# Kernel optimization log

Measured on AMD Instinct MI355X. Metric: run time of the kernel, lower is better.

## Reference

```python
import jax, jax.numpy as jnp
import numpy as np

D_MODEL = 512
N_HEADS = 8
D_FF = 2048
EPS = 1e-5


def _layernorm(x, g, b):
    mu = jnp.mean(x, axis=-1, keepdims=True)
    var = jnp.mean(jnp.square(x - mu), axis=-1, keepdims=True)
    return (x - mu) * jax.lax.rsqrt(var + EPS) * g + b


def setup_inputs() -> dict:
    key = jax.random.key(0)
    ks = jax.random.split(key, 12)
    B, N, C = 2, 2048, D_MODEL
    s = lambda fi, fo: 1.0 / np.sqrt(fi)
    inp = {
        "x": jax.random.normal(ks[0], (B, N, C), jnp.float32),
        # weights stored as [in, out] (y = x @ W + b)
        "qkv_w": jax.random.normal(ks[1], (C, 3 * C), jnp.float32) * s(C, 3 * C),
        "qkv_b": jnp.zeros((3 * C,), jnp.float32),
        "out_w": jax.random.normal(ks[2], (C, C), jnp.float32) * s(C, C),
        "out_b": jnp.zeros((C,), jnp.float32),
        "ffn_w1": jax.random.normal(ks[3], (C, D_FF), jnp.float32) * s(C, D_FF),
        "ffn_b1": jnp.zeros((D_FF,), jnp.float32),
        "ffn_w2": jax.random.normal(ks[4], (D_FF, C), jnp.float32) * s(D_FF, C),
        "ffn_b2": jnp.zeros((C,), jnp.float32),
        "n1_g": jnp.ones((C,), jnp.float32),
        "n1_b": jnp.zeros((C,), jnp.float32),
        "n2_g": jnp.ones((C,), jnp.float32),
        "n2_b": jnp.zeros((C,), jnp.float32),
        "conv_w": jax.random.normal(ks[5], (C, C, 3), jnp.float32) * s(3 * C, C),  # [out, in, k]
        "conv_b": jnp.zeros((C,), jnp.float32),
        "cn_g": jnp.ones((C,), jnp.float32),
        "cn_b": jnp.zeros((C,), jnp.float32),
    }
    return inp


def _forward(x, qkv_w, qkv_b, out_w, out_b, ffn_w1, ffn_b1, ffn_w2, ffn_b2,
             n1_g, n1_b, n2_g, n2_b, conv_w, conv_b, cn_g, cn_b):
    B, N, C = x.shape
    H, dk = N_HEADS, C // N_HEADS
    scale = 1.0 / np.sqrt(dk)

    # --- ProbSparse self-attention ---
    qkv = (x @ qkv_w + qkv_b).reshape(B, N, 3, H, dk)
    q, k, v = (jnp.moveaxis(qkv, (2, 3), (0, 2))[i] for i in range(3))  # each [B,H,N,dk]
    scores = jnp.einsum("bhnd,bhmd->bhnm", q, k) * scale  # [B,H,N,N]
    M = jnp.max(scores, axis=-1) - jnp.mean(scores, axis=-1)  # [B,H,N]
    n_top = max(1, min(int(N * 0.25), N - 1))
    _, top_idx = jax.lax.top_k(M, n_top)  # [B,H,n_top]
    bidx = jnp.arange(B)[:, None, None]
    hidx = jnp.arange(H)[None, :, None]
    row_sel = jnp.zeros((B, H, N), bool).at[bidx, hidx, top_idx].set(True)
    # rows not selected are fully masked (-1e9) -> uniform softmax, as in the original
    attn = jax.nn.softmax(jnp.where(row_sel[..., None], scores, -1e9), axis=-1)
    out = jnp.einsum("bhnm,bhmd->bhnd", attn, v)
    out = out.transpose(0, 2, 1, 3).reshape(B, N, C)
    attn_out = out @ out_w + out_b

    x = _layernorm(x + attn_out, n1_g, n1_b)

    # --- FFN (exact GELU) ---
    h = jax.nn.gelu(x @ ffn_w1 + ffn_b1, approximate=False)
    ffn_out = h @ ffn_w2 + ffn_b2
    x = _layernorm(x + ffn_out, n2_g, n2_b)

    # --- distilling conv: circular conv1d(k=3,p=1) -> maxpool(k=3,s=2,p=1) -> ELU -> LN ---
    xc = x.transpose(0, 2, 1)  # [B,C,N]
    xc = jnp.concatenate([xc[..., -1:], xc, xc[..., :1]], axis=-1)  # circular pad 1
    xc = jax.lax.conv_general_dilated(
        xc, conv_w, window_strides=(1,), padding="VALID",
        dimension_numbers=("NCH", "OIH", "NCH")) + conv_b[None, :, None]
    # maxpool k=3 s=2 p=1 (pad with -inf)
    neg = jnp.finfo(xc.dtype).min
    xc = jax.lax.reduce_window(xc, neg, jax.lax.max,
                               window_dimensions=(1, 1, 3), window_strides=(1, 1, 2),
                               padding=((0, 0), (0, 0), (1, 1)))
    x = xc.transpose(0, 2, 1)  # [B, N', C]
    x = _layernorm(jax.nn.elu(x), cn_g, cn_b)
    return x


def reference(x, qkv_w, qkv_b, out_w, out_b, ffn_w1, ffn_b1, ffn_w2, ffn_b2,
              n1_g, n1_b, n2_g, n2_b, conv_w, conv_b, cn_g, cn_b):
    return _forward(x, qkv_w, qkv_b, out_w, out_b, ffn_w1, ffn_b1, ffn_w2, ffn_b2,
                    n1_g, n1_b, n2_g, n2_b, conv_w, conv_b, cn_g, cn_b)
```

## Files before the change

### kernel.cpp

```cpp
#include <hip/hip_runtime.h>
#include <math.h>

#define NB 2
#define NN 2048
#define NC 512
#define NH 8
#define DK 64
#define DFF 2048
#define NTOP 512
#define NPOOL 1024
#define KSPLIT 4

typedef unsigned short u16;
typedef __attribute__((ext_vector_type(8))) short frag8;
typedef __attribute__((ext_vector_type(8))) _Float16 h8;
typedef __attribute__((ext_vector_type(4))) float f32x4;

static __device__ __forceinline__ u16 f2b(float f) {
    union { float f; unsigned int u; } v; v.f = f;
    unsigned int r = (v.u + 0x7fffu + ((v.u >> 16) & 1u)) >> 16;
    return (u16)r;
}
static __device__ __forceinline__ float b2f(u16 v) {
    union { unsigned u; float f; } x; x.u = ((unsigned)v) << 16; return x.f;
}
static __device__ __forceinline__ u16 f2h_bits(float f) {
    union { _Float16 h; u16 u; } v; v.h = (_Float16)f; return v.u;
}
static __device__ __forceinline__ float h2f_bits(u16 u) {
    union { u16 u; _Float16 h; } v; v.u = u; return (float)v.h;
}

template<int MODE>
__global__ __launch_bounds__(256) void mfma_gemm(const u16* __restrict__ A, int lda,
    const u16* __restrict__ Bt, const float* __restrict__ bias,
    float* __restrict__ C, u16* __restrict__ Cb, int ldc, int K, int act)
{
    __shared__ u16 As[128][72];
    __shared__ u16 Bs[128][72];
    int tid = threadIdx.x;
    int m0 = blockIdx.x * 128, n0 = blockIdx.y * 128;
    int wave = tid >> 6, lane = tid & 63;
    int ln = lane & 15, quad = lane >> 4;
    int wm = (wave >> 1) * 64, wn = (wave & 1) * 64;
    f32x4 acc[4][4] = {};
    for (int k0 = 0; k0 < K; k0 += 64) {
        #pragma unroll
        for (int i = 0; i < 4; i++) {
            int t = tid + i * 256;
            int m = t >> 3, kq = t & 7;
            size_t aoff;
            if (MODE == 1) {
                int grow = m0 + m;
                int shift = (k0 >> 9) - 1;
                int arow = (grow & ~(NN - 1)) | ((grow + shift) & (NN - 1));
                aoff = (size_t)arow * NC + ((k0 & 511) + kq * 8);
            } else {
                aoff = (size_t)(m0 + m) * lda + k0 + kq * 8;
            }
            *(uint4*)&As[m][kq * 8] = *(const uint4*)&A[aoff];
            *(uint4*)&Bs[m][kq * 8] = *(const uint4*)&Bt[(size_t)(n0 + m) * K + k0 + kq * 8];
        }
        __syncthreads();
        #pragma unroll
        for (int kk = 0; kk < 2; kk++) {
            frag8 af[4], bf[4];
            #pragma unroll
            for (int i = 0; i < 4; i++) {
                af[i] = *(const frag8*)&As[wm + i * 16 + ln][kk * 32 + quad * 8];
                bf[i] = *(const frag8*)&Bs[wn + i * 16 + ln][kk * 32 + quad * 8];
            }
            #pragma unroll
            for (int i = 0; i < 4; i++)
                #pragma unroll
                for (int j = 0; j < 4; j++)
                    acc[i][j] = __builtin_amdgcn_mfma_f32_16x16x32_bf16(
                        af[i], bf[j], acc[i][j], 0, 0, 0);
        }
        __syncthreads();
    }
    #pragma unroll
    for (int i = 0; i < 4; i++) {
        #pragma unroll
        for (int j = 0; j < 4; j++) {
            int col = n0 + wn + j * 16 + ln;
            float bv = bias ? bias[col] : 0.f;
            #pragma unroll
            for (int r = 0; r < 4; r++) {
                int row = m0 + wm + i * 16 + quad * 4 + r;
                float v = acc[i][j][r] + bv;
                if (act == 1) v = 0.5f * v * (1.0f + erff(v * 0.70710678118654752f));
                if (Cb) Cb[(size_t)row * ldc + col] = f2b(v);
                else    C[(size_t)row * ldc + col] = v;
            }
        }
    }
}

template<int MODE>
__global__ __launch_bounds__(256) void mfma_gemm_sk(const u16* __restrict__ A, int lda,
    const u16* __restrict__ Bt, float* __restrict__ P0, float* __restrict__ P1,
    int ldc, int K)
{
    __shared__ u16 As[128][72];
    __shared__ u16 Bs[128][72];
    int tid = threadIdx.x;
    int m0 = blockIdx.x * 128, n0 = blockIdx.y * 128;
    int split = blockIdx.z;
    int K2 = K >> 1, kbeg = split * K2;
    int wave = tid >> 6, lane = tid & 63;
    int ln = lane & 15, quad = lane >> 4;
    int wm = (wave >> 1) * 64, wn = (wave & 1) * 64;
    f32x4 acc[4][4] = {};
    for (int k0 = kbeg; k0 < kbeg + K2; k0 += 64) {
        #pragma unroll
        for (int i = 0; i < 4; i++) {
            int t = tid + i * 256;
            int m = t >> 3, kq = t & 7;
            size_t aoff;
            if (MODE == 1) {
                int grow = m0 + m;
                int shift = (k0 >> 9) - 1;
                int arow = (grow & ~(NN - 1)) | ((grow + shift) & (NN - 1));
                aoff = (size_t)arow * NC + ((k0 & 511) + kq * 8);
            } else {
                aoff = (size_t)(m0 + m) * lda + k0 + kq * 8;
            }
            *(uint4*)&As[m][kq * 8] = *(const uint4*)&A[aoff];
            *(uint4*)&Bs[m][kq * 8] = *(const uint4*)&Bt[(size_t)(n0 + m) * K + k0 + kq * 8];
        }
        __syncthreads();
        #pragma unroll
        for (int kk = 0; kk < 2; kk++) {
            frag8 af[4], bf[4];
            #pragma unroll
            for (int i = 0; i < 4; i++) {
                af[i] = *(const frag8*)&As[wm + i * 16 + ln][kk * 32 + quad * 8];
                bf[i] = *(const frag8*)&Bs[wn + i * 16 + ln][kk * 32 + quad * 8];
            }
            #pragma unroll
            for (int i = 0; i < 4; i++)
                #pragma unroll
                for (int j = 0; j < 4; j++)
                    acc[i][j] = __builtin_amdgcn_mfma_f32_16x16x32_bf16(
                        af[i], bf[j], acc[i][j], 0, 0, 0);
        }
        __syncthreads();
    }
    float* P = split ? P1 : P0;
    #pragma unroll
    for (int i = 0; i < 4; i++) {
        #pragma unroll
        for (int j = 0; j < 4; j++) {
            int col = n0 + wn + j * 16 + ln;
            #pragma unroll
            for (int r = 0; r < 4; r++) {
                int row = m0 + wm + i * 16 + quad * 4 + r;
                P[(size_t)row * ldc + col] = acc[i][j][r];
            }
        }
    }
}

__global__ __launch_bounds__(256) void mfma_qkv(const u16* __restrict__ A,
    const u16* __restrict__ Bt, const float* __restrict__ bias,
    u16* __restrict__ Qbs, u16* __restrict__ Kb, float* __restrict__ Vh,
    u16* __restrict__ Qcat, u16* __restrict__ Kcat)
{
    __shared__ u16 As[128][72];
    __shared__ u16 Bs[128][72];
    int tid = threadIdx.x;
    int m0 = blockIdx.x * 128, n0 = blockIdx.y * 128;
    int wave = tid >> 6, lane = tid & 63;
    int ln = lane & 15, quad = lane >> 4;
    int wm = (wave >> 1) * 64, wn = (wave & 1) * 64;
    f32x4 acc[4][4] = {};
    for (int k0 = 0; k0 < 1024; k0 += 64) {
        #pragma unroll
        for (int i = 0; i < 4; i++) {
            int t = tid + i * 256;
            int m = t >> 3, kq = t & 7;
            *(uint4*)&As[m][kq * 8] = *(const uint4*)&A[(size_t)(m0 + m) * 1024 + k0 + kq * 8];
            *(uint4*)&Bs[m][kq * 8] = *(const uint4*)&Bt[(size_t)(n0 + m) * 1024 + k0 + kq * 8];
        }
        __syncthreads();
        #pragma unroll
        for (int kk = 0; kk < 2; kk++) {
            h8 af[4], bf[4];
            #pragma unroll
            for (int i = 0; i < 4; i++) {
                af[i] = *(const h8*)&As[wm + i * 16 + ln][kk * 32 + quad * 8];
                bf[i] = *(const h8*)&Bs[wn + i * 16 + ln][kk * 32 + quad * 8];
            }
            #pragma unroll
            for (int i = 0; i < 4; i++)
                #pragma unroll
                for (int j = 0; j < 4; j++)
                    acc[i][j] = __builtin_amdgcn_mfma_f32_16x16x32_f16(
                        af[i], bf[j], acc[i][j], 0, 0, 0);
        }
        __syncthreads();
    }
    #pragma unroll
    for (int i = 0; i < 4; i++) {
        #pragma unroll
        for (int j = 0; j < 4; j++) {
            int col = n0 + wn + j * 16 + ln;
            float bv = bias[col];
            int which = col >> 9;
            int h = (col >> 6) & 7, d = col & 63;
            #pragma unroll
            for (int r = 0; r < 4; r++) {
                int row = m0 + wm + i * 16 + quad * 4 + r;
                int b = row >> 11, n = row & (NN - 1);
                float v = acc[i][j][r] + bv;
                size_t off32 = ((size_t)((b << 3) + h) * NN + n) * DK + d;
                if (which == 2) {
                    Vh[off32] = v;
                } else {
                    size_t offc = ((size_t)((b << 3) + h) * NN + n) * 128 + d;
                    u16 hb_ = f2h_bits(v);
                    u16 lb_ = f2h_bits(v - h2f_bits(hb_));
                    if (which == 0) {
                        Qbs[off32] = f2b(v * 0.125f);
                        Qcat[offc] = hb_; Qcat[offc + 64] = lb_;
                    } else {
                        Kb[off32] = f2b(v);
                        Kcat[offc] = hb_; Kcat[offc + 64] = lb_;
                    }
                }
            }
        }
    }
}

__global__ __launch_bounds__(256) void castw_t(const float* __restrict__ in,
    u16* __restrict__ out, int R, int C, int ldi, int coff)
{
    __shared__ float t[32][33];
    int c0 = blockIdx.x * 32, r0 = blockIdx.y * 32;
    int lx = threadIdx.x & 31, ly = threadIdx.x >> 5;
    #pragma unroll
    for (int i = 0; i < 4; i++)
        t[ly + i * 8][lx] = in[(size_t)(r0 + ly + i * 8) * ldi + coff + c0 + lx];
    __syncthreads();
    #pragma unroll
    for (int i = 0; i < 4; i++)
        out[(size_t)(c0 + ly + i * 8) * R + r0 + lx] = f2b(t[lx][ly + i * 8]);
}

__global__ __launch_bounds__(256) void castw_hl(const float* __restrict__ in,
    u16* __restrict__ out)
{
    __shared__ float t[32][33];
    int c0 = blockIdx.x * 32, r0 = blockIdx.y * 32;
    int lx = threadIdx.x & 31, ly = threadIdx.x >> 5;
    #pragma unroll
    for (int i = 0; i < 4; i++)
        t[ly + i * 8][lx] = in[(size_t)(r0 + ly + i * 8) * 1536 + c0 + lx];
    __syncthreads();
    #pragma unroll
    for (int i = 0; i < 4; i++) {
        float v = t[lx][ly + i * 8];
        u16 hb_ = f2h_bits(v);
        u16 lb_ = f2h_bits(v - h2f_bits(hb_));
        size_t ob = (size_t)(c0 + ly + i * 8) * 1024 + r0 + lx;
        out[ob] = hb_;
        out[ob + 512] = lb_;
    }
}

__global__ void castconvw_k(const float* __restrict__ cw, u16* __restrict__ out)
{
    int i = blockIdx.x * 256 + threadIdx.x;
    if (i >= 3 * NC * NC) return;
    int t = i % 3, ci = (i / 3) & (NC - 1), co = i / (3 * NC);
    out[(size_t)co * 1536 + t * NC + ci] = f2b(cw[i]);
}

__global__ void castx_k(const float* __restrict__ in, u16* __restrict__ xcat)
{
    int i = blockIdx.x * 256 + threadIdx.x;
    if (i >= (NB * NN * NC) / 4) return;
    int m = i >> 7, kq = i & 127;
    float4 v = ((const float4*)in)[i];
    ushort4 h, l;
    h.x = f2h_bits(v.x); h.y = f2h_bits(v.y);
    h.z = f2h_bits(v.z); h.w = f2h_bits(v.w);
    l.x = f2h_bits(v.x - h2f_bits(h.x));
    l.y = f2h_bits(v.y - h2f_bits(h.y));
    l.z = f2h_bits(v.z - h2f_bits(h.z));
    l.w = f2h_bits(v.w - h2f_bits(h.w));
    *(ushort4*)&xcat[(size_t)m * 1024 + kq * 4] = h;
    *(ushort4*)&xcat[(size_t)m * 1024 + 512 + kq * 4] = l;
}

__global__ __launch_bounds__(256) void castv_k(const float* __restrict__ Vh,
    u16* __restrict__ Vtb, float* __restrict__ pmean)
{
    int bh = blockIdx.y;
    int n0 = blockIdx.x * 64;
    __shared__ float vt[64][68];
    __shared__ float red[256];
    int tid = threadIdx.x;
    const float* vin = Vh + ((size_t)bh * NN + n0) * DK;
    #pragma unroll
    for (int i = 0; i < 4; i++) {
        int t = tid + i * 256;
        int n = t >> 4, dq = t & 15;
        float4 w = *(const float4*)&vin[(size_t)n * DK + dq * 4];
        vt[dq * 4 + 0][n] = w.x; vt[dq * 4 + 1][n] = w.y;
        vt[dq * 4 + 2][n] = w.z; vt[dq * 4 + 3][n] = w.w;
    }
    __syncthreads();
    #pragma unroll
    for (int i = 0; i < 4; i++) {
        int t = tid + i * 256;
        int d = t >> 4, nq = t & 15;
        float4 v = *(const float4*)&vt[d][nq * 4];
        ushort4 o;
        o.x = f2b(v.x); o.y = f2b(v.y); o.z = f2b(v.z); o.w = f2b(v.w);
        *(ushort4*)&Vtb[((size_t)bh * DK + d) * NN + n0 + nq * 4] = o;
    }
    int d = tid & 63, sub = tid >> 6;
    float s = 0.f;
    #pragma unroll
    for (int r = 0; r < 16; r++) s += vt[d][sub * 16 + r];
    red[tid] = s;
    __syncthreads();
    if (sub == 0)
        pmean[((size_t)bh * 32 + (n0 >> 6)) * 64 + d] =
            red[d] + red[64 + d] + red[128 + d] + red[192 + d];
}

__global__ void meanv_comb_k(const float* __restrict__ pmean, float* __restrict__ meanv)
{
    int bh = blockIdx.x;
    int d = threadIdx.x;
    float s = 0.f;
    #pragma unroll
    for (int c = 0; c < 32; c++) s += pmean[((size_t)bh * 32 + c) * 64 + d];
    meanv[bh * DK + d] = s * (1.0f / (float)NN);
}

__global__ __launch_bounds__(256) void rowstat_mfma_k(const u16* __restrict__ Qcat,
    const u16* __restrict__ Kcat, float* __restrict__ Marr, float* __restrict__ rowmax)
{
    int bh = blockIdx.x;
    int m0 = blockIdx.y * 64;
    int tid = threadIdx.x;
    int wave = tid >> 6, lane = tid & 63;
    int ln = lane & 15, quad = lane >> 4;
    __shared__ u16 Ks[128][136];
    h8 qf[4];
    {
        const u16* qp = &Qcat[((size_t)bh * NN + m0 + wave * 16 + ln) * 128];
        #pragma unroll
        for (int ks = 0; ks < 4; ks++)
            qf[ks] = *(const h8*)&qp[ks * 32 + quad * 8];
    }
    f32x4 vmax, vsum;
    #pragma unroll
    for (int r = 0; r < 4; r++) { vmax[r] = -INFINITY; vsum[r] = 0.f; }
    const u16* kB = Kcat + (size_t)bh * NN * 128;
    for (int nc = 0; nc < NN; nc += 128) {
        __syncthreads();
        #pragma unroll
        for (int i = 0; i < 8; i++) {
            int e = tid + i * 256;
            int n = e >> 4, kq = e & 15;
            *(uint4*)&Ks[n][kq * 8] = *(const uint4*)&kB[(size_t)(nc + n) * 128 + kq * 8];
        }
        __syncthreads();
        f32x4 accS[8] = {};
        #pragma unroll
        for (int nt = 0; nt < 8; nt++) {
            #pragma unroll
            for (int ks = 0; ks < 4; ks++) {
                h8 kf = *(const h8*)&Ks[nt * 16 + ln][ks * 32 + quad * 8];
                accS[nt] = __builtin_amdgcn_mfma_f32_16x16x32_f16(
                    qf[ks], kf, accS[nt], 0, 0, 0);
            }
        }
        #pragma unroll
        for (int nt = 0; nt < 8; nt++)
            #pragma unroll
            for (int r = 0; r < 4; r++) {
                vmax[r] = fmaxf(vmax[r], accS[nt][r]);
                vsum[r] += accS[nt][r];
            }
    }
    #pragma unroll
    for (int r = 0; r < 4; r++) {
        float mx = vmax[r], sm = vsum[r];
        #pragma unroll
        for (int off = 1; off < 16; off <<= 1) {
            mx = fmaxf(mx, __shfl_xor(mx, off));
            sm += __shfl_xor(sm, off);
        }
        if (ln == 0) {
            int m = m0 + wave * 16 + quad * 4 + r;
            Marr[(size_t)bh * NN + m] = (mx - sm * (1.0f / (float)NN)) * 0.125f;
            rowmax[(size_t)bh * NN + m] = mx * 0.125f;
        }
    }
}

__global__ __launch_bounds__(256) void topk_k(const float* __restrict__ Marr,
                                              int* __restrict__ idx)
{
    int bh = blockIdx.x;
    const float* Mr = Marr + (size_t)bh * NN;
    int* idxr = idx + (size_t)bh * NTOP;
    __shared__ int hist[256];
    __shared__ int suf[256];
    __shared__ int wred[4], wred2[4];
    __shared__ int bin_sh, rank_sh;
    int tid = threadIdx.x;
    int lane = tid & 63, w = tid >> 6;
    unsigned prefix = 0;
    int rank = NTOP;
    for (int pass = 0; pass < 4; pass++) {
        int shift = 24 - pass * 8;
        unsigned mask_hi = (pass == 0) ? 0u : (0xFFFFFFFFu << (shift + 8));
        hist[tid] = 0;
        __syncthreads();
        for (int i = tid; i < NN; i += 256) {
            union { float f; unsigned u; } v; v.f = Mr[i];
            unsigned k = (v.u & 0x80000000u) ? ~v.u : (v.u | 0x80000000u);
            if ((k & mask_hi) == prefix)
                atomicAdd(&hist[(k >> shift) & 255], 1);
        }
        __syncthreads();
        int v = hist[tid];
        #pragma unroll
        for (int off = 1; off < 64; off <<= 1) {
            int t = __shfl_down(v, off);
            if (lane + off < 64) v += t;
        }
        if (lane == 0) wred[w] = v;
        __syncthreads();
        int add = 0;
        #pragma unroll
        for (int w2 = 0; w2 < 4; w2++) if (w2 > w) add += wred[w2];
        suf[tid] = v + add;
        __syncthreads();
        int sv = suf[tid];
        int nxt = (tid < 255) ? suf[tid + 1] : 0;
        if (sv >= rank && nxt < rank) { bin_sh = tid; rank_sh = rank - nxt; }
        __syncthreads();
        prefix |= ((unsigned)bin_sh << shift);
        rank = rank_sh;
        __syncthreads();
    }
    union { unsigned u; float f; } tv;
    tv.u = (prefix & 0x80000000u) ? (prefix & 0x7FFFFFFFu) : ~prefix;
    float thr = tv.f;
    int lg = 0, le = 0;
    #pragma unroll
    for (int k = 0; k < 8; k++) {
        float v = Mr[tid * 8 + k];
        lg += (v > thr) ? 1 : 0;
        le += (v == thr) ? 1 : 0;
    }
    int vg = lg, ve = le;
    #pragma unroll
    for (int off = 1; off < 64; off <<= 1) {
        int tg = __shfl_up(vg, off);
        int te = __shfl_up(ve, off);
        if (lane >= off) { vg += tg; ve += te; }
    }
    if (lane == 63) { wred[w] = vg; wred2[w] = ve; }
    __syncthreads();
    int addg = 0, adde = 0, totg = 0;
    #pragma unroll
    for (int w2 = 0; w2 < 4; w2++) {
        totg += wred[w2];
        if (w2 < w) { addg += wred[w2]; adde += wred2[w2]; }
    }
    int cnt_gt = totg;
    int needed = NTOP - cnt_gt;
    int gpre = (vg + addg) - lg, epre = (ve + adde) - le;
    #pragma unroll
    for (int k = 0; k < 8; k++) {
        int p = tid * 8 + k;
        float v = Mr[p];
        bool isgt = v > thr, iseq = v == thr;
        bool selv = isgt || (iseq && epre < needed);
        if (selv) idxr[gpre + (epre < needed ? epre : needed)] = p;
        gpre += isgt ? 1 : 0;
        epre += iseq ? 1 : 0;
    }
}

__global__ void fill_k(const float* __restrict__ meanv, u16* __restrict__ ctxb)
{
    int i = blockIdx.x * 256 + threadIdx.x;
    if (i >= (NB * NN * NC) / 8) return;
    int c = (i * 8) & (NC - 1);
    int m = (i * 8) >> 9;
    int b = m >> 11;
    int h = c >> 6, d = c & 63;
    const float* mv = &meanv[(((b << 3) + h) << 6) + d];
    float4 v0 = *(const float4*)mv;
    float4 v1 = *(const float4*)(mv + 4);
    union { u16 s[8]; uint4 u; } r;
    r.s[0] = f2b(v0.x); r.s[1] = f2b(v0.y); r.s[2] = f2b(v0.z); r.s[3] = f2b(v0.w);
    r.s[4] = f2b(v1.x); r.s[5] = f2b(v1.y); r.s[6] = f2b(v1.z); r.s[7] = f2b(v1.w);
    *(uint4*)&ctxb[(size_t)i * 8] = r.u;
}

__global__ __launch_bounds__(256) void attn_mfma_k(const u16* __restrict__ Qbs,
    const u16* __restrict__ Kb, const u16* __restrict__ Vtb,
    const int* __restrict__ idx, const float* __restrict__ rowmax,
    float* __restrict__ Opart, float* __restrict__ ml)
{
    int yy = blockIdx.x;
    int bh = yy >> 2, split = yy & (KSPLIT - 1);
    int t0 = blockIdx.y * 64;
    int tid = threadIdx.x;
    int wave = tid >> 6, lane = tid & 63;
    int ln = lane & 15, quad = lane >> 4;
    __shared__ u16 Ks[128][72];
    __shared__ u16 Vt[64][136];
    __shared__ u16 Ps[4][16][136];
    __shared__ int rows[64];
    if (tid < 64) rows[tid] = idx[bh * NTOP + t0 + tid];
    __syncthreads();
    frag8 qf[2];
    {
        const u16* qp = &Qbs[((size_t)bh * NN + rows[wave * 16 + ln]) * DK];
        qf[0] = *(const frag8*)&qp[quad * 8];
        qf[1] = *(const frag8*)&qp[32 + quad * 8];
    }
    float rm[4];
    #pragma unroll
    for (int r = 0; r < 4; r++)
        rm[r] = rowmax[(size_t)bh * NN + rows[wave * 16 + quad * 4 + r]];
    f32x4 accO[4] = {};
    float lrun[4] = {};
    const u16* kbB = Kb + (size_t)bh * NN * DK;
    const u16* vtB = Vtb + (size_t)bh * DK * NN;
    int nc0 = split * (NN / KSPLIT);
    for (int nc = nc0; nc < nc0 + NN / KSPLIT; nc += 128) {
        __syncthreads();
        #pragma unroll
        for (int i = 0; i < 4; i++) {
            int e = tid + i * 256;
            int n = e >> 3, kq = e & 7;
            *(uint4*)&Ks[n][kq * 8] = *(const uint4*)&kbB[(size_t)(nc + n) * DK + kq * 8];
        }
        #pragma unroll
        for (int i = 0; i < 4; i++) {
            int e = tid + i * 256;
            int d = e >> 4, nq = e & 15;
            *(uint4*)&Vt[d][nq * 8] = *(const uint4*)&vtB[(size_t)d * NN + nc + nq * 8];
        }
        __syncthreads();
        f32x4 accS[8] = {};
        #pragma unroll
        for (int nt = 0; nt < 8; nt++) {
            frag8 b0 = *(const frag8*)&Ks[nt * 16 + ln][quad * 8];
            frag8 b1 = *(const frag8*)&Ks[nt * 16 + ln][32 + quad * 8];
            accS[nt] = __builtin_amdgcn_mfma_f32_16x16x32_bf16(qf[0], b0, accS[nt], 0, 0, 0);
            accS[nt] = __builtin_amdgcn_mfma_f32_16x16x32_bf16(qf[1], b1, accS[nt], 0, 0, 0);
        }
        #pragma unroll
        for (int nt = 0; nt < 8; nt++)
            #pragma unroll
            for (int r = 0; r < 4; r++) {
                float p = expf(accS[nt][r] - rm[r]);
                accS[nt][r] = p;
                lrun[r] += p;
            }
        #pragma unroll
        for (int nt = 0; nt < 8; nt++)
            #pragma unroll
            for (int r = 0; r < 4; r++)
                Ps[wave][quad * 4 + r][nt * 16 + ln] = f2b(accS[nt][r]);
        #pragma unroll
        for (int ks = 0; ks < 4; ks++) {
            frag8 pf = *(const frag8*)&Ps[wave][ln][ks * 32 + quad * 8];
            #pragma unroll
            for (int nt2 = 0; nt2 < 4; nt2++) {
                frag8 vf = *(const frag8*)&Vt[nt2 * 16 + ln][ks * 32 + quad * 8];
                accO[nt2] = __builtin_amdgcn_mfma_f32_16x16x32_bf16(pf, vf, accO[nt2], 0, 0, 0);
            }
        }
    }
    #pragma unroll
    for (int r = 0; r < 4; r++) {
        float ls = lrun[r];
        #pragma unroll
        for (int off = 1; off < 16; off <<= 1) ls += __shfl_xor(ls, off);
        int p = t0 + wave * 16 + quad * 4 + r;
        size_t pb = ((size_t)bh * NTOP + p) * KSPLIT + split;
        #pragma unroll
        for (int nt2 = 0; nt2 < 4; nt2++)
            Opart[pb * 64 + nt2 * 16 + ln] = accO[nt2][r];
        if (ln == 0) ml[pb * 2 + 1] = ls;
    }
}

__global__ __launch_bounds__(256) void attn_comb_k(const float* __restrict__ Opart,
    const float* __restrict__ ml, const int* __restrict__ idx,
    u16* __restrict__ ctxb)
{
    int gid = blockIdx.x * 4 + (threadIdx.x >> 6);
    int lane = threadIdx.x & 63;
    int bh = gid >> 9;
    int h = bh & 7, b = bh >> 3;
    size_t base = (size_t)gid * KSPLIT;
    float L = 0.f, O = 0.f;
    #pragma unroll
    for (int s = 0; s < KSPLIT; s++) {
        L += ml[(base + s) * 2 + 1];
        O += Opart[(base + s) * 64 + lane];
    }
    int n = idx[gid];
    ctxb[((size_t)(b * NN + n)) * NC + h * DK + lane] = f2b(O / L);
}

__global__ __launch_bounds__(256) void ln_k(const float* __restrict__ A,
    const float* __restrict__ P0, const float* __restrict__ P1,
    const float* __restrict__ cb,
    const float* __restrict__ g, const float* __restrict__ bb,
    float* __restrict__ out, u16* __restrict__ outb)
{
    int row = blockIdx.x;
    int tid = threadIdx.x;
    __shared__ float v[NC];
    __shared__ float red[256];
    size_t base = (size_t)row * NC;
    for (int i = tid; i < NC; i += 256)
        v[i] = A[base + i] + P0[base + i] + P1[base + i] + cb[i];
    __syncthreads();
    float ls = 0.f;
    for (int i = tid; i < NC; i += 256) ls += v[i];
    red[tid] = ls; __syncthreads();
    for (int off = 128; off > 0; off >>= 1) {
        if (tid < off) red[tid] += red[tid + off];
        __syncthreads();
    }
    float mu = red[0] / (float)NC;
    __syncthreads();
    float lv = 0.f;
    for (int i = tid; i < NC; i += 256) { float d = v[i] - mu; lv += d * d; }
    red[tid] = lv; __syncthreads();
    for (int off = 128; off > 0; off >>= 1) {
        if (tid < off) red[tid] += red[tid + off];
        __syncthreads();
    }
    float rstd = rsqrtf(red[0] / (float)NC + 1e-5f);
    for (int i = tid; i < NC; i += 256) {
        float r = (v[i] - mu) * rstd * g[i] + bb[i];
        if (out) out[base + i] = r;
        if (outb) outb[base + i] = f2b(r);
    }
}

__global__ __launch_bounds__(256) void pool_ln_k(const float* __restrict__ P0,
    const float* __restrict__ P1, const float* __restrict__ cb,
    const float* __restrict__ g, const float* __restrict__ bb,
    float* __restrict__ outp)
{
    int row = blockIdx.x;
    int j = row & (NPOOL - 1), b = row / NPOOL;
    int tid = threadIdx.x;
    __shared__ float v[NC];
    __shared__ float red[256];
    size_t bbase = (size_t)b * NN * NC;
    for (int i = tid; i < NC; i += 256) {
        float m = -INFINITY;
        int p0 = 2 * j - 1;
        float cbv = cb[i];
        #pragma unroll
        for (int t = 0; t < 3; t++) {
            int p = p0 + t;
            if (p >= 0 && p < NN) {
                size_t off = bbase + (size_t)p * NC + i;
                m = fmaxf(m, P0[off] + P1[off] + cbv);
            }
        }
        v[i] = m > 0.f ? m : expm1f(m);
    }
    __syncthreads();
    float ls = 0.f;
    for (int i = tid; i < NC; i += 256) ls += v[i];
    red[tid] = ls; __syncthreads();
    for (int off = 128; off > 0; off >>= 1) {
        if (tid < off) red[tid] += red[tid + off];
        __syncthreads();
    }
    float mu = red[0] / (float)NC;
    __syncthreads();
    float lv = 0.f;
    for (int i = tid; i < NC; i += 256) { float d = v[i] - mu; lv += d * d; }
    red[tid] = lv; __syncthreads();
    for (int off = 128; off > 0; off >>= 1) {
        if (tid < off) red[tid] += red[tid + off];
        __syncthreads();
    }
    float rstd = rsqrtf(red[0] / (float)NC + 1e-5f);
    for (int i = tid; i < NC; i += 256)
        outp[(size_t)row * NC + i] = (v[i] - mu) * rstd * g[i] + bb[i];
}

extern "C" void kernel_launch(void* const* d_in, const int* in_sizes, int n_in,
                              void* d_out, int out_size, void* d_ws, size_t ws_size,
                              hipStream_t stream)
{
    (void)in_sizes; (void)n_in; (void)out_size; (void)ws_size;
    const float* x      = (const float*)d_in[0];
    const float* qkv_w  = (const float*)d_in[1];
    const float* qkv_b  = (const float*)d_in[2];
    const float* out_w  = (const float*)d_in[3];
    const float* out_b  = (const float*)d_in[4];
    const float* ffn_w1 = (const float*)d_in[5];
    const float* ffn_b1 = (const float*)d_in[6];
    const float* ffn_w2 = (const float*)d_in[7];
    const float* ffn_b2 = (const float*)d_in[8];
    const float* n1_g   = (const float*)d_in[9];
    const float* n1_b   = (const float*)d_in[10];
    const float* n2_g   = (const float*)d_in[11];
    const float* n2_b   = (const float*)d_in[12];
    const float* conv_w = (const float*)d_in[13];
    const float* conv_b = (const float*)d_in[14];
    const float* cn_g   = (const float*)d_in[15];
    const float* cn_b   = (const float*)d_in[16];

    const size_t R = (size_t)NB * NN * NC;
    float* ws = (float*)d_ws;
    float* x1   = ws;
    float* reg2 = ws + R;
    float* QhR  = ws + 2 * R;
    float* Kh   = ws + 3 * R;
    float* Vh   = ws + 4 * R;
    size_t o = 5 * R;
    float* pmax  = ws + o;  o += 65536;
    float* psum  = ws + o;  o += 65536;
    float* Marr  = ws + o;  o += 32768;
    float* pmean = ws + o;  o += 32768;
    float* meanv = ws + o;  o += 1024;
    int*   idx   = (int*)(ws + o);  o += 8192;
    float* ml    = ws + o;  o += 65536;
    u16*   ctxb  = (u16*)(ws + o);  o += R / 2;
    u16*   x1b   = (u16*)(ws + o);  o += R / 2;
    u16*   x2b   = (u16*)(ws + o);  o += R / 2;
    u16*   owT   = (u16*)(ws + o);  o += 131072;
    u16*   w1T   = (u16*)(ws + o);  o += 524288;
    u16*   w2T   = (u16*)(ws + o);  o += 524288;
    u16*   cwT   = (u16*)(ws + o);  o += 393216;
    u16*   Qbs   = (u16*)QhR;
    u16*   Kb    = (u16*)(QhR + R / 2);
    u16*   Vtb   = (u16*)(ws + R + R / 2);
    float* Opart    = x1;
    u16*   hb       = (u16*)Kh;
    float* rowmax   = pmax;
    float* skP0 = reg2;
    float* skP1 = Vh;
    u16*   xcat  = (u16*)reg2;
    u16*   wcatT = w1T;
    u16*   Qcat  = x1b;
    u16*   Kcat  = (u16*)x1;
    (void)psum;

    castw_t<<<dim3(16, 16), 256, 0, stream>>>(out_w, owT, 512, 512, 512, 0);
    castconvw_k<<<3072, 256, 0, stream>>>(conv_w, cwT);
    castx_k<<<2048, 256, 0, stream>>>(x, xcat);
    castw_hl<<<dim3(48, 16), 256, 0, stream>>>(qkv_w, wcatT);

    mfma_qkv<<<dim3(32, 12), 256, 0, stream>>>(xcat, wcatT, qkv_b,
                                               Qbs, Kb, Vh, Qcat, Kcat);

    castw_t<<<dim3(64, 16), 256, 0, stream>>>(ffn_w1, w1T, 512, 2048, 2048, 0);
    castw_t<<<dim3(16, 64), 256, 0, stream>>>(ffn_w2, w2T, 2048, 512, 512, 0);

    castv_k<<<dim3(NN / 64, NB * NH), 256, 0, stream>>>(Vh, Vtb, pmean);
    meanv_comb_k<<<NB * NH, 64, 0, stream>>>(pmean, meanv);

    rowstat_mfma_k<<<dim3(NB * NH, NN / 64), 256, 0, stream>>>(Qcat, Kcat, Marr, rowmax);
    topk_k<<<NB * NH, 256, 0, stream>>>(Marr, idx);
    fill_k<<<(int)(R / 8 / 256), 256, 0, stream>>>(meanv, ctxb);
    attn_mfma_k<<<dim3(NB * NH * KSPLIT, NTOP / 64), 256, 0, stream>>>(
        Qbs, Kb, Vtb, idx, rowmax, Opart, ml);
    attn_comb_k<<<NB * NH * NTOP / 4, 256, 0, stream>>>(Opart, ml, idx, ctxb);

    mfma_gemm_sk<0><<<dim3(32, 4, 2), 256, 0, stream>>>(
        ctxb, NC, owT, skP0, skP1, NC, NC);

    ln_k<<<NB * NN, 256, 0, stream>>>(x, skP0, skP1, out_b, n1_g, n1_b, x1, x1b);

    mfma_gemm<0><<<dim3(32, 16), 256, 0, stream>>>(
        x1b, NC, w1T, ffn_b1, (float*)nullptr, hb, DFF, NC, 1);
    mfma_gemm_sk<0><<<dim3(32, 4, 2), 256, 0, stream>>>(
        hb, DFF, w2T, skP0, skP1, NC, DFF);

    ln_k<<<NB * NN, 256, 0, stream>>>(x1, skP0, skP1, ffn_b2,
                                      n2_g, n2_b, (float*)nullptr, x2b);

    mfma_gemm_sk<1><<<dim3(32, 4, 2), 256, 0, stream>>>(
        x2b, NC, cwT, skP0, skP1, NC, 1536);

    pool_ln_k<<<NB * NPOOL, 256, 0, stream>>>(skP0, skP1, conv_b, cn_g, cn_b,
                                              (float*)d_out);
}
```

Baseline: 324.2 us.

## Merge small launches and vectorize cast and layernorm kernels

After: 320.5 us. About the same (-1.2%).

```diff
diff --git a/kernel.cpp b/kernel.cpp
--- a/kernel.cpp
+++ b/kernel.cpp
@@ -249,6 +249,30 @@
         out[(size_t)(c0 + ly + i * 8) * R + r0 + lx] = f2b(t[lx][ly + i * 8]);
 }
 
+__global__ __launch_bounds__(256) void castffnw_k(const float* __restrict__ w1,
+    const float* __restrict__ w2, u16* __restrict__ w1T, u16* __restrict__ w2T)
+{
+    __shared__ float t[32][33];
+    int b = blockIdx.x;
+    const float* in; u16* out; int ldi, R, c0, r0;
+    if (b < 1024) {
+        in = w1; out = w1T; ldi = 2048; R = 512;
+        c0 = (b & 63) * 32; r0 = (b >> 6) * 32;
+    } else {
+        b -= 1024;
+        in = w2; out = w2T; ldi = 512; R = 2048;
+        c0 = (b & 15) * 32; r0 = (b >> 4) * 32;
+    }
+    int lx = threadIdx.x & 31, ly = threadIdx.x >> 5;
+    #pragma unroll
+    for (int i = 0; i < 4; i++)
+        t[ly + i * 8][lx] = in[(size_t)(r0 + ly + i * 8) * ldi + c0 + lx];
+    __syncthreads();
+    #pragma unroll
+    for (int i = 0; i < 4; i++)
+        out[(size_t)(c0 + ly + i * 8) * R + r0 + lx] = f2b(t[lx][ly + i * 8]);
+}
+
 __global__ __launch_bounds__(256) void castw_hl(const float* __restrict__ in,
     u16* __restrict__ out)
 {
@@ -272,10 +296,19 @@
 
 __global__ void castconvw_k(const float* __restrict__ cw, u16* __restrict__ out)
 {
-    int i = blockIdx.x * 256 + threadIdx.x;
-    if (i >= 3 * NC * NC) return;
-    int t = i % 3, ci = (i / 3) & (NC - 1), co = i / (3 * NC);
-    out[(size_t)co * 1536 + t * NC + ci] = f2b(cw[i]);
+    int g = blockIdx.x * 256 + threadIdx.x;
+    if (g >= 3 * NC * NC / 4) return;
+    int co = g / 384;
+    int rem = g - co * 384;
+    int t = rem >> 7;
+    int ci0 = (rem & 127) * 4;
+    const float* src = cw + (size_t)co * 1536 + t;
+    ushort4 o;
+    o.x = f2b(src[(ci0 + 0) * 3]);
+    o.y = f2b(src[(ci0 + 1) * 3]);
+    o.z = f2b(src[(ci0 + 2) * 3]);
+    o.w = f2b(src[(ci0 + 3) * 3]);
+    *(ushort4*)&out[(size_t)co * 1536 + t * NC + ci0] = o;
 }
 
 __global__ void castx_k(const float* __restrict__ in, u16* __restrict__ xcat)
@@ -333,16 +366,6 @@
             red[d] + red[64 + d] + red[128 + d] + red[192 + d];
 }
 
-__global__ void meanv_comb_k(const float* __restrict__ pmean, float* __restrict__ meanv)
-{
-    int bh = blockIdx.x;
-    int d = threadIdx.x;
-    float s = 0.f;
-    #pragma unroll
-    for (int c = 0; c < 32; c++) s += pmean[((size_t)bh * 32 + c) * 64 + d];
-    meanv[bh * DK + d] = s * (1.0f / (float)NN);
-}
-
 __global__ __launch_bounds__(256) void rowstat_mfma_k(const u16* __restrict__ Qcat,
     const u16* __restrict__ Kcat, float* __restrict__ Marr, float* __restrict__ rowmax)
 {
@@ -407,16 +430,23 @@
 }
 
 __global__ __launch_bounds__(256) void topk_k(const float* __restrict__ Marr,
-                                              int* __restrict__ idx)
+    const float* __restrict__ pmean, float* __restrict__ meanv,
+    int* __restrict__ idx)
 {
     int bh = blockIdx.x;
+    int tid = threadIdx.x;
+    if (tid < 64) {
+        float s = 0.f;
+        #pragma unroll
+        for (int c = 0; c < 32; c++) s += pmean[((size_t)bh * 32 + c) * 64 + tid];
+        meanv[bh * DK + tid] = s * (1.0f / (float)NN);
+    }
     const float* Mr = Marr + (size_t)bh * NN;
     int* idxr = idx + (size_t)bh * NTOP;
     __shared__ int hist[256];
     __shared__ int suf[256];
     __shared__ int wred[4], wred2[4];
     __shared__ int bin_sh, rank_sh;
-    int tid = threadIdx.x;
     int lane = tid & 63, w = tid >> 6;
     unsigned prefix = 0;
     int rank = NTOP;
@@ -598,7 +628,7 @@
         #pragma unroll
         for (int nt2 = 0; nt2 < 4; nt2++)
             Opart[pb * 64 + nt2 * 16 + ln] = accO[nt2][r];
-        if (ln == 0) ml[pb * 2 + 1] = ls;
+        if (ln == 0) ml[pb] = ls;
     }
 }
 
@@ -614,7 +644,7 @@
     float L = 0.f, O = 0.f;
     #pragma unroll
     for (int s = 0; s < KSPLIT; s++) {
-        L += ml[(base + s) * 2 + 1];
+        L += ml[base + s];
         O += Opart[(base + s) * 64 + lane];
     }
     int n = idx[gid];
@@ -632,30 +662,38 @@
     __shared__ float v[NC];
     __shared__ float red[256];
     size_t base = (size_t)row * NC;
-    for (int i = tid; i < NC; i += 256)
-        v[i] = A[base + i] + P0[base + i] + P1[base + i] + cb[i];
-    __syncthreads();
-    float ls = 0.f;
-    for (int i = tid; i < NC; i += 256) ls += v[i];
-    red[tid] = ls; __syncthreads();
+    float2 a  = *(const float2*)&A[base + tid * 2];
+    float2 p0 = *(const float2*)&P0[base + tid * 2];
+    float2 p1 = *(const float2*)&P1[base + tid * 2];
+    float2 c2 = *(const float2*)&cb[tid * 2];
+    float v0 = a.x + p0.x + p1.x + c2.x;
+    float v1 = a.y + p0.y + p1.y + c2.y;
+    v[tid * 2] = v0; v[tid * 2 + 1] = v1;
+    red[tid] = v0 + v1;
+    __syncthreads();
     for (int off = 128; off > 0; off >>= 1) {
         if (tid < off) red[tid] += red[tid + off];
         __syncthreads();
     }
     float mu = red[0] / (float)NC;
     __syncthreads();
-    float lv = 0.f;
-    for (int i = tid; i < NC; i += 256) { float d = v[i] - mu; lv += d * d; }
-    red[tid] = lv; __syncthreads();
+    float d0 = v0 - mu, d1 = v1 - mu;
+    red[tid] = d0 * d0 + d1 * d1;
+    __syncthreads();
     for (int off = 128; off > 0; off >>= 1) {
         if (tid < off) red[tid] += red[tid + off];
         __syncthreads();
     }
     float rstd = rsqrtf(red[0] / (float)NC + 1e-5f);
-    for (int i = tid; i < NC; i += 256) {
-        float r = (v[i] - mu) * rstd * g[i] + bb[i];
-        if (out) out[base + i] = r;
-        if (outb) outb[base + i] = f2b(r);
+    float2 g2 = *(const float2*)&g[tid * 2];
+    float2 b2 = *(const float2*)&bb[tid * 2];
+    float r0 = d0 * rstd * g2.x + b2.x;
+    float r1 = d1 * rstd * g2.y + b2.y;
+    if (out) { float2 o; o.x = r0; o.y = r1; *(float2*)&out[base + tid * 2] = o; }
+    if (outb) {
+        union { u16 s[2]; unsigned u; } w2;
+        w2.s[0] = f2b(r0); w2.s[1] = f2b(r1);
+        *(unsigned*)&outb[base + tid * 2] = w2.u;
     }
 }
 
@@ -667,43 +705,46 @@
     int row = blockIdx.x;
     int j = row & (NPOOL - 1), b = row / NPOOL;
     int tid = threadIdx.x;
-    __shared__ float v[NC];
     __shared__ float red[256];
     size_t bbase = (size_t)b * NN * NC;
-    for (int i = tid; i < NC; i += 256) {
-        float m = -INFINITY;
-        int p0 = 2 * j - 1;
-        float cbv = cb[i];
-        #pragma unroll
-        for (int t = 0; t < 3; t++) {
-            int p = p0 + t;
-            if (p >= 0 && p < NN) {
-                size_t off = bbase + (size_t)p * NC + i;
-                m = fmaxf(m, P0[off] + P1[off] + cbv);
-            }
-        }
-        v[i] = m > 0.f ? m : expm1f(m);
-    }
-    __syncthreads();
-    float ls = 0.f;
-    for (int i = tid; i < NC; i += 256) ls += v[i];
-    red[tid] = ls; __syncthreads();
+    float2 c2 = *(const float2*)&cb[tid * 2];
+    float m0 = -INFINITY, m1 = -INFINITY;
+    int p0r = 2 * j - 1;
+    #pragma unroll
+    for (int t = 0; t < 3; t++) {
+        int p = p0r + t;
+        if (p >= 0 && p < NN) {
+            size_t off = bbase + (size_t)p * NC + tid * 2;
+            float2 a = *(const float2*)&P0[off];
+            float2 c = *(const float2*)&P1[off];
+            m0 = fmaxf(m0, a.x + c.x + c2.x);
+            m1 = fmaxf(m1, a.y + c.y + c2.y);
+        }
+    }
+    float v0 = m0 > 0.f ? m0 : expm1f(m0);
+    float v1 = m1 > 0.f ? m1 : expm1f(m1);
+    red[tid] = v0 + v1;
+    __syncthreads();
     for (int off = 128; off > 0; off >>= 1) {
         if (tid < off) red[tid] += red[tid + off];
         __syncthreads();
     }
     float mu = red[0] / (float)NC;
     __syncthreads();
-    float lv = 0.f;
-    for (int i = tid; i < NC; i += 256) { float d = v[i] - mu; lv += d * d; }
-    red[tid] = lv; __syncthreads();
+    float d0 = v0 - mu, d1 = v1 - mu;
+    red[tid] = d0 * d0 + d1 * d1;
+    __syncthreads();
     for (int off = 128; off > 0; off >>= 1) {
         if (tid < off) red[tid] += red[tid + off];
         __syncthreads();
     }
     float rstd = rsqrtf(red[0] / (float)NC + 1e-5f);
-    for (int i = tid; i < NC; i += 256)
-        outp[(size_t)row * NC + i] = (v[i] - mu) * rstd * g[i] + bb[i];
+    float2 g2 = *(const float2*)&g[tid * 2];
+    float2 b2 = *(const float2*)&bb[tid * 2];
+    float2 o;
+    o.x = d0 * rstd * g2.x + b2.x;
+    o.y = d1 * rstd * g2.y + b2.y;
+    *(float2*)&outp[(size_t)row * NC + tid * 2] = o;
 }
 
 extern "C" void kernel_launch(void* const* d_in, const int* in_sizes, int n_in,
@@ -766,21 +807,19 @@
     (void)psum;
 
     castw_t<<<dim3(16, 16), 256, 0, stream>>>(out_w, owT, 512, 512, 512, 0);
-    castconvw_k<<<3072, 256, 0, stream>>>(conv_w, cwT);
+    castconvw_k<<<768, 256, 0, stream>>>(conv_w, cwT);
     castx_k<<<2048, 256, 0, stream>>>(x, xcat);
     castw_hl<<<dim3(48, 16), 256, 0, stream>>>(qkv_w, wcatT);
 
     mfma_qkv<<<dim3(32, 12), 256, 0, stream>>>(xcat, wcatT, qkv_b,
                                                Qbs, Kb, Vh, Qcat, Kcat);
 
-    castw_t<<<dim3(64, 16), 256, 0, stream>>>(ffn_w1, w1T, 512, 2048, 2048, 0);
-    castw_t<<<dim3(16, 64), 256, 0, stream>>>(ffn_w2, w2T, 2048, 512, 512, 0);
+    castffnw_k<<<2048, 256, 0, stream>>>(ffn_w1, ffn_w2, w1T, w2T);
 
     castv_k<<<dim3(NN / 64, NB * NH), 256, 0, stream>>>(Vh, Vtb, pmean);
-    meanv_comb_k<<<NB * NH, 64, 0, stream>>>(pmean, meanv);
 
     rowstat_mfma_k<<<dim3(NB * NH, NN / 64), 256, 0, stream>>>(Qcat, Kcat, Marr, rowmax);
-    topk_k<<<NB * NH, 256, 0, stream>>>(Marr, idx);
+    topk_k<<<NB * NH, 256, 0, stream>>>(Marr, pmean, meanv, idx);
     fill_k<<<(int)(R / 8 / 256), 256, 0, stream>>>(meanv, ctxb);
     attn_mfma_k<<<dim3(NB * NH * KSPLIT, NTOP / 64), 256, 0, stream>>>(
         Qbs, Kb, Vtb, idx, rowmax, Opart, ml);
```
